# Performance work log

Measured on AMD Instinct MI355X. Metric: run time of the kernel, lower is better.

The kernel has to match this reference:

```python
import jax, jax.numpy as jnp
import numpy as np

B, S, D, H, DH = 4, 2048, 512, 8, 64

def setup_inputs() -> dict:
    key = jax.random.key(0)
    k1, k2, k3, k4 = jax.random.split(key, 4)
    sc = 1.0 / np.sqrt(D)
    return {
        "x": jax.random.normal(k1, (B, S, D), dtype=jnp.float32),
        "Wq": jax.random.normal(k2, (H, D, DH), dtype=jnp.float32) * sc,
        "Wk": jax.random.normal(k3, (H, D, DH), dtype=jnp.float32) * sc,
        "Wv": jax.random.normal(k4, (H, D, DH), dtype=jnp.float32) * sc,
    }

def reference(x, Wq, Wk, Wv):
    # x: [B,S,D]; Wq/Wk/Wv: [H,D,DH] (stacked per-head bias-free Linear weights)
    q = jnp.einsum('bsd,hdk->bhsk', x, Wq)
    k = jnp.einsum('bsd,hdk->bhsk', x, Wk)
    v = jnp.einsum('bsd,hdk->bhsk', x, Wv)
    scale = DH ** -0.5
    scores = jax.nn.softmax(jnp.einsum('bhqk,bhsk->bhqs', q, k) * scale, axis=-1)
    out = jnp.einsum('bhqs,bhsk->bhqk', scores, v)  # [B,H,S,DH]
    # concat heads along last dim (head order matches ModuleList order)
    return out.transpose(0, 2, 1, 3).reshape(B, S, H * DH)
```

## Files before the change

### kernel.cpp

```cpp
#include <hip/hip_runtime.h>

typedef _Float16 half8  __attribute__((ext_vector_type(8)));
typedef _Float16 half4v __attribute__((ext_vector_type(4)));
typedef _Float16 half2v __attribute__((ext_vector_type(2)));
typedef __fp16   fp16x2 __attribute__((ext_vector_type(2)));
typedef float    float4v __attribute__((ext_vector_type(4)));

#define CSC 0.18033688f

__device__ __forceinline__ void async16(const _Float16* g, void* l) {
    __builtin_amdgcn_global_load_lds((const __attribute__((address_space(1))) void*)g,
                                     (__attribute__((address_space(3))) void*)l, 16, 0, 0);
}

__device__ __forceinline__ half2v pk2(float a, float b) {
    return __builtin_bit_cast(half2v, __builtin_amdgcn_cvt_pkrtz(a, b));
}

__global__ __launch_bounds__(256) void mha_prep(const float* __restrict__ x,
    const float* __restrict__ wq, const float* __restrict__ wk, const float* __restrict__ wv,
    _Float16* __restrict__ xh, _Float16* __restrict__ wt) {
    __shared__ __align__(16) _Float16 T[64][72];
    const int tid = threadIdx.x;
    if (blockIdx.x < 4096) {
        int t = blockIdx.x * 256 + tid;
        float4v v = ((const float4v*)x)[t];
        half4v o;
        #pragma unroll
        for (int i = 0; i < 4; ++i) o[i] = (_Float16)v[i];
        ((half4v*)xh)[t] = o;
        return;
    }
    const int blk = blockIdx.x - 4096;
    const int dt = blk & 7, h = (blk >> 3) & 7, mat = blk >> 6;
    const float* w = ((mat == 0) ? wq : (mat == 1) ? wk : wv) + h * 32768 + dt * 64 * 64;
    #pragma unroll
    for (int i = 0; i < 4; ++i) {
        int s = tid + i * 256;
        int dl = s >> 4, c4 = s & 15;
        float4v v = ((const float4v*)(w + (size_t)dl * 64))[c4];
        #pragma unroll
        for (int e = 0; e < 4; ++e) T[c4 * 4 + e][dl] = (_Float16)v[e];
    }
    __syncthreads();
    #pragma unroll
    for (int i = 0; i < 2; ++i) {
        int s = tid + i * 256;
        int dh = s >> 3, c8 = s & 7;
        half8 o;
        #pragma unroll
        for (int e = 0; e < 8; ++e) o[e] = T[dh][c8 * 8 + e];
        *(half8*)(wt + (size_t)((mat * 8 + h) * 64 + dh) * 512 + dt * 64 + c8 * 8) = o;
    }
}

__global__ __launch_bounds__(256, 3) void mha_qkv(const _Float16* __restrict__ xh,
    const _Float16* __restrict__ wt, _Float16* __restrict__ Qm, _Float16* __restrict__ Km,
    _Float16* __restrict__ Vt) {
    __shared__ __align__(16) _Float16 Ash[2][128 * 32];
    __shared__ __align__(16) _Float16 Bsh[2][128 * 32];
    const int tid = threadIdx.x;
    const int lane = tid & 63, wave = tid >> 6;
    const int quad = lane >> 4, li = lane & 15;
    const int m0 = blockIdx.x * 128, n0 = blockIdx.y * 128;
    float4v acc[4][4] = {};
    const int r0 = tid >> 2, c0 = (tid & 3) ^ ((r0 >> 1) & 3);
    const int s1 = 256 + tid, r1 = s1 >> 2, c1 = (s1 & 3) ^ ((r1 >> 1) & 3);
    const _Float16* gA0 = xh + (size_t)(m0 + r0) * 512 + c0 * 8;
    const _Float16* gA1 = xh + (size_t)(m0 + r1) * 512 + c1 * 8;
    const _Float16* gB0 = wt + (size_t)(n0 + r0) * 512 + c0 * 8;
    const _Float16* gB1 = wt + (size_t)(n0 + r1) * 512 + c1 * 8;
    const int wr = (wave >> 1) * 64, wc = (wave & 1) * 64;
    const char* aB[2]; const char* bB[2];
    #pragma unroll
    for (int bb = 0; bb < 2; ++bb) {
        aB[bb] = (const char*)Ash[bb] + (wr + li) * 64 + ((quad ^ ((li >> 1) & 3)) << 4);
        bB[bb] = (const char*)Bsh[bb] + (wc + li) * 64 + ((quad ^ ((li >> 1) & 3)) << 4);
    }
    auto stage = [&](int bb, int kk) {
        async16(gA0 + kk, (char*)Ash[bb] + wave * 1024);
        async16(gA1 + kk, (char*)Ash[bb] + 4096 + wave * 1024);
        async16(gB0 + kk, (char*)Bsh[bb] + wave * 1024);
        async16(gB1 + kk, (char*)Bsh[bb] + 4096 + wave * 1024);
    };
    auto compute = [&](int bb) {
        half8 af[4], bf[4];
        #pragma unroll
        for (int mt = 0; mt < 4; ++mt) af[mt] = *(const half8*)(aB[bb] + mt * 1024);
        #pragma unroll
        for (int nt = 0; nt < 4; ++nt) bf[nt] = *(const half8*)(bB[bb] + nt * 1024);
        #pragma unroll
        for (int mt = 0; mt < 4; ++mt)
            #pragma unroll
            for (int nt = 0; nt < 4; ++nt)
                acc[mt][nt] = __builtin_amdgcn_mfma_f32_16x16x32_f16(af[mt], bf[nt], acc[mt][nt], 0, 0, 0);
    };
    stage(0, 0);
    for (int kk = 0; kk < 512; kk += 64) {
        __syncthreads();
        stage(1, kk + 32);
        compute(0);
        __syncthreads();
        if (kk + 64 < 512) stage(0, kk + 64);
        compute(1);
    }
    const int mat = n0 >> 9;
    const float osc = (mat == 0) ? CSC : 1.0f;
    #pragma unroll
    for (int mt = 0; mt < 4; ++mt) {
        int m = m0 + wr + mt * 16 + quad * 4;
        int b = m >> 11, s = m & 2047;
        #pragma unroll
        for (int nt = 0; nt < 4; ++nt) {
            int n = n0 + wc + nt * 16 + li;
            int h = (n >> 6) & 7, dh = n & 63;
            int bh = b * 8 + h;
            if (mat == 2) {
                half4v pkv;
                #pragma unroll
                for (int r = 0; r < 4; ++r) pkv[r] = (_Float16)acc[mt][nt][r];
                *(half4v*)(Vt + ((size_t)bh * 64 + dh) * 2048 + s) = pkv;
            } else {
                _Float16* dst = (mat == 0) ? Qm : Km;
                size_t base = ((size_t)bh * 2048 + s) * 64 + dh;
                #pragma unroll
                for (int r = 0; r < 4; ++r) dst[base + (size_t)r * 64] = (_Float16)(acc[mt][nt][r] * osc);
            }
        }
    }
}

__global__ __launch_bounds__(128, 2) void mha_attn(const _Float16* __restrict__ Qm,
    const _Float16* __restrict__ Km, const _Float16* __restrict__ Vt, float* __restrict__ out) {
    __shared__ __align__(16) _Float16 KtA[2][64 * 64];
    __shared__ __align__(16) _Float16 VtA[2][64 * 64];
    const int tid = threadIdx.x, lane = tid & 63, wave = tid >> 6;
    const int quad = lane >> 4, li = lane & 15;
    const int flat = blockIdx.x;
    const int qb = (flat >> 3) & 31;
    const int bh = ((flat >> 8) << 3) | (flat & 7);
    const int b = bh >> 3, h = bh & 7;
    const _Float16* Qg = Qm + (size_t)bh * 2048 * 64;
    const _Float16* Kg = Km + (size_t)bh * 2048 * 64;
    const _Float16* Vg = Vt + (size_t)bh * 64 * 2048;
    const int q0 = qb * 64 + wave * 32;
    half8 qf[2][2];
    #pragma unroll
    for (int qt = 0; qt < 2; ++qt)
        #pragma unroll
        for (int ds = 0; ds < 2; ++ds)
            qf[qt][ds] = *(const half8*)(Qg + (size_t)(q0 + qt * 16 + li) * 64 + ds * 32 + quad * 8);
    float4v O[2][4] = {};
    float lsum[2] = {0.f, 0.f};
    const _Float16* pK[4]; const _Float16* pV[4];
    #pragma unroll
    for (int is = 0; is < 4; ++is) {
        int s = is * 128 + tid;
        int rk = s >> 3, sck = s & 7;
        int swk = (rk & 3) | (((rk >> 3) & 1) << 2);
        int rv = s >> 3, cv = (s & 7) ^ (rv & 7);
        pK[is] = Kg + (size_t)rk * 64 + (sck ^ swk) * 8;
        pV[is] = Vg + (size_t)rv * 2048 + cv * 8;
    }
    auto stage = [&](int bb) {
        #pragma unroll
        for (int is = 0; is < 4; ++is) {
            async16(pK[is], (char*)KtA[bb] + is * 2048 + wave * 1024);
            async16(pV[is], (char*)VtA[bb] + is * 2048 + wave * 1024);
            pK[is] += 4096;
            pV[is] += 64;
        }
    };
    const int rowE = ((li >> 2) << 3) | (li & 3);
    const int swzE = (li & 3) | (((li >> 2) & 1) << 2);
    const char *k0e[2], *k1e[2], *vBq[2];
    #pragma unroll
    for (int bb = 0; bb < 2; ++bb) {
        const char* base = (const char*)KtA[bb] + rowE * 128;
        k0e[bb] = base + ((quad ^ swzE) << 4);
        k1e[bb] = base + (((quad + 4) ^ swzE) << 4);
        vBq[bb] = (const char*)VtA[bb] + li * 128;
    }
    int coff[2];
    #pragma unroll
    for (int c = 0; c < 2; ++c) coff[c] = (((c * 4 + quad) ^ (li & 7)) << 4);
    auto compute = [&](int bb) {
        #pragma unroll
        for (int c = 0; c < 2; ++c) {
            half8 f0e = *(const half8*)(k0e[bb] + c * 4096);
            half8 f1e = *(const half8*)(k1e[bb] + c * 4096);
            half8 f0o = *(const half8*)(k0e[bb] + c * 4096 + 512);
            half8 f1o = *(const half8*)(k1e[bb] + c * 4096 + 512);
            float4v se[2] = {}, so[2] = {};
            se[0] = __builtin_amdgcn_mfma_f32_16x16x32_f16(f0e, qf[0][0], se[0], 0, 0, 0);
            se[0] = __builtin_amdgcn_mfma_f32_16x16x32_f16(f1e, qf[0][1], se[0], 0, 0, 0);
            se[1] = __builtin_amdgcn_mfma_f32_16x16x32_f16(f0e, qf[1][0], se[1], 0, 0, 0);
            se[1] = __builtin_amdgcn_mfma_f32_16x16x32_f16(f1e, qf[1][1], se[1], 0, 0, 0);
            so[0] = __builtin_amdgcn_mfma_f32_16x16x32_f16(f0o, qf[0][0], so[0], 0, 0, 0);
            so[0] = __builtin_amdgcn_mfma_f32_16x16x32_f16(f1o, qf[0][1], so[0], 0, 0, 0);
            so[1] = __builtin_amdgcn_mfma_f32_16x16x32_f16(f0o, qf[1][0], so[1], 0, 0, 0);
            so[1] = __builtin_amdgcn_mfma_f32_16x16x32_f16(f1o, qf[1][1], so[1], 0, 0, 0);
            half8 pf[2];
            #pragma unroll
            for (int qt = 0; qt < 2; ++qt) {
                float pe[4], po[4];
                #pragma unroll
                for (int r = 0; r < 4; ++r) {
                    pe[r] = __builtin_amdgcn_exp2f(se[qt][r]);
                    po[r] = __builtin_amdgcn_exp2f(so[qt][r]);
                    lsum[qt] += pe[r] + po[r];
                }
                half4v a = __builtin_shufflevector(pk2(pe[0], pe[1]), pk2(pe[2], pe[3]), 0, 1, 2, 3);
                half4v o = __builtin_shufflevector(pk2(po[0], po[1]), pk2(po[2], po[3]), 0, 1, 2, 3);
                pf[qt] = __builtin_shufflevector(a, o, 0, 1, 2, 3, 4, 5, 6, 7);
            }
            #pragma unroll
            for (int dt = 0; dt < 4; ++dt) {
                half8 vf = *(const half8*)(vBq[bb] + dt * 2048 + coff[c]);
                O[0][dt] = __builtin_amdgcn_mfma_f32_16x16x32_f16(pf[0], vf, O[0][dt], 0, 0, 0);
                O[1][dt] = __builtin_amdgcn_mfma_f32_16x16x32_f16(pf[1], vf, O[1][dt], 0, 0, 0);
            }
        }
    };
    stage(0);
    for (int it = 0; it < 16; ++it) {
        __syncthreads();
        stage(1);
        compute(0);
        __syncthreads();
        if (it < 15) stage(0);
        compute(1);
    }
    #pragma unroll
    for (int qt = 0; qt < 2; ++qt) {
        float l = lsum[qt];
        l += __shfl_xor(l, 16);
        l += __shfl_xor(l, 32);
        #pragma unroll
        for (int r = 0; r < 4; ++r) {
            float lr = __shfl(l, quad * 4 + r);
            float inv = 1.0f / lr;
            int q = q0 + qt * 16 + quad * 4 + r;
            float* orow = out + ((size_t)(b * 2048 + q)) * 512 + h * 64;
            #pragma unroll
            for (int dt = 0; dt < 4; ++dt) orow[dt * 16 + li] = O[qt][dt][r] * inv;
        }
    }
}

extern "C" void kernel_launch(void* const* d_in, const int* in_sizes, int n_in,
                              void* d_out, int out_size, void* d_ws, size_t ws_size,
                              hipStream_t stream) {
    const float* x  = (const float*)d_in[0];
    const float* wq = (const float*)d_in[1];
    const float* wk = (const float*)d_in[2];
    const float* wv = (const float*)d_in[3];
    float* out = (float*)d_out;
    char* ws = (char*)d_ws;
    _Float16* xh = (_Float16*)(ws);
    _Float16* wt = (_Float16*)(ws + 8388608);
    _Float16* Qm = (_Float16*)(ws + 9961472);
    _Float16* Km = (_Float16*)(ws + 18350080);
    _Float16* Vt = (_Float16*)(ws + 26738688);
    if (ws_size < 35127296u) return;
    mha_prep<<<4288, 256, 0, stream>>>(x, wq, wk, wv, xh, wt);
    mha_qkv<<<dim3(64, 12), 256, 0, stream>>>(xh, wt, Qm, Km, Vt);
    mha_attn<<<1024, 128, 0, stream>>>(Qm, Km, Vt, out);
}
```

Baseline: 144.2 us.

## Split attention keys across two blocks with flag-based combine; stage Q/K epilogue via LDS

The attention kernel now uses 256-thread blocks covering 128 queries. Each block handles half of the key sequence. It writes unnormalized partial outputs and row sums to workspace, and the second block to finish (detected with an atomic counter) merges both halves and normalizes. Separately, the QKV GEMM epilogue for Q and K goes through an LDS transpose so the global stores are 16-byte vectors instead of scattered 2-byte writes. The split costs extra partial-output traffic, a memset and atomics. It relies on no max subtraction, since the scores are never shifted before exp2.

```diff
diff --git a/kernel.cpp b/kernel.cpp
--- a/kernel.cpp
+++ b/kernel.cpp
@@ -57,8 +57,9 @@
 __global__ __launch_bounds__(256, 3) void mha_qkv(const _Float16* __restrict__ xh,
     const _Float16* __restrict__ wt, _Float16* __restrict__ Qm, _Float16* __restrict__ Km,
     _Float16* __restrict__ Vt) {
-    __shared__ __align__(16) _Float16 Ash[2][128 * 32];
-    __shared__ __align__(16) _Float16 Bsh[2][128 * 32];
+    __shared__ __align__(16) char smem[34816];
+    _Float16* Ash[2] = { (_Float16*)smem,           (_Float16*)(smem + 8192)  };
+    _Float16* Bsh[2] = { (_Float16*)(smem + 16384), (_Float16*)(smem + 24576) };
     const int tid = threadIdx.x;
     const int lane = tid & 63, wave = tid >> 6;
     const int quad = lane >> 4, li = lane & 15;
@@ -105,45 +106,71 @@
         compute(1);
     }
     const int mat = n0 >> 9;
-    const float osc = (mat == 0) ? CSC : 1.0f;
-    #pragma unroll
-    for (int mt = 0; mt < 4; ++mt) {
-        int m = m0 + wr + mt * 16 + quad * 4;
-        int b = m >> 11, s = m & 2047;
-        #pragma unroll
-        for (int nt = 0; nt < 4; ++nt) {
-            int n = n0 + wc + nt * 16 + li;
-            int h = (n >> 6) & 7, dh = n & 63;
-            int bh = b * 8 + h;
-            if (mat == 2) {
+    if (mat == 2) {
+        #pragma unroll
+        for (int mt = 0; mt < 4; ++mt) {
+            int m = m0 + wr + mt * 16 + quad * 4;
+            int b = m >> 11, s = m & 2047;
+            #pragma unroll
+            for (int nt = 0; nt < 4; ++nt) {
+                int n = n0 + wc + nt * 16 + li;
+                int h = (n >> 6) & 7, dh = n & 63;
+                int bh = b * 8 + h;
                 half4v pkv;
                 #pragma unroll
                 for (int r = 0; r < 4; ++r) pkv[r] = (_Float16)acc[mt][nt][r];
                 *(half4v*)(Vt + ((size_t)bh * 64 + dh) * 2048 + s) = pkv;
-            } else {
-                _Float16* dst = (mat == 0) ? Qm : Km;
-                size_t base = ((size_t)bh * 2048 + s) * 64 + dh;
+            }
+        }
+    } else {
+        _Float16* dst = (mat == 0) ? Qm : Km;
+        const float osc = (mat == 0) ? CSC : 1.0f;
+        __syncthreads();
+        char* Tb = smem;
+        #pragma unroll
+        for (int mt = 0; mt < 4; ++mt) {
+            int rbase = wr + mt * 16 + quad * 4;
+            #pragma unroll
+            for (int nt = 0; nt < 4; ++nt) {
+                int col = wc + nt * 16 + li;
                 #pragma unroll
-                for (int r = 0; r < 4; ++r) dst[base + (size_t)r * 64] = (_Float16)(acc[mt][nt][r] * osc);
+                for (int r = 0; r < 4; ++r)
+                    *(_Float16*)(Tb + (rbase + r) * 272 + col * 2) = (_Float16)(acc[mt][nt][r] * osc);
             }
         }
-    }
-}
-
-__global__ __launch_bounds__(128, 2) void mha_attn(const _Float16* __restrict__ Qm,
-    const _Float16* __restrict__ Km, const _Float16* __restrict__ Vt, float* __restrict__ out) {
+        __syncthreads();
+        const int h0 = (n0 >> 6) & 7;
+        #pragma unroll
+        for (int i = 0; i < 8; ++i) {
+            int c = i * 256 + tid;
+            int row = c >> 4, j8 = c & 15;
+            half8 v = *(const half8*)(Tb + row * 272 + j8 * 16);
+            int m = m0 + row;
+            int b = m >> 11, s = m & 2047;
+            int bh = b * 8 + h0 + (j8 >> 3);
+            *(half8*)(dst + ((size_t)bh * 2048 + s) * 64 + (j8 & 7) * 8) = v;
+        }
+    }
+}
+
+__global__ __launch_bounds__(256, 4) void mha_attn(const _Float16* __restrict__ Qm,
+    const _Float16* __restrict__ Km, const _Float16* __restrict__ Vt,
+    float* __restrict__ opart, float* __restrict__ lpart, int* __restrict__ flags,
+    float* __restrict__ out) {
     __shared__ __align__(16) _Float16 KtA[2][64 * 64];
     __shared__ __align__(16) _Float16 VtA[2][64 * 64];
+    __shared__ int sflag;
     const int tid = threadIdx.x, lane = tid & 63, wave = tid >> 6;
     const int quad = lane >> 4, li = lane & 15;
     const int flat = blockIdx.x;
-    const int qb = (flat >> 3) & 31;
+    const int qb = (flat >> 3) & 15;
+    const int ks = (flat >> 7) & 1;
     const int bh = ((flat >> 8) << 3) | (flat & 7);
     const int b = bh >> 3, h = bh & 7;
     const _Float16* Qg = Qm + (size_t)bh * 2048 * 64;
-    const _Float16* Kg = Km + (size_t)bh * 2048 * 64;
-    const _Float16* Vg = Vt + (size_t)bh * 64 * 2048;
-    const int q0 = qb * 64 + wave * 32;
+    const _Float16* Kg = Km + (size_t)bh * 2048 * 64 + (size_t)ks * 1024 * 64;
+    const _Float16* Vg = Vt + (size_t)bh * 64 * 2048 + (size_t)ks * 1024;
+    const int q0 = qb * 128 + wave * 32;
     half8 qf[2][2];
     #pragma unroll
     for (int qt = 0; qt < 2; ++qt)
@@ -152,21 +179,21 @@
             qf[qt][ds] = *(const half8*)(Qg + (size_t)(q0 + qt * 16 + li) * 64 + ds * 32 + quad * 8);
     float4v O[2][4] = {};
     float lsum[2] = {0.f, 0.f};
-    const _Float16* pK[4]; const _Float16* pV[4];
-    #pragma unroll
-    for (int is = 0; is < 4; ++is) {
-        int s = is * 128 + tid;
-        int rk = s >> 3, sck = s & 7;
+    const _Float16* pK[2]; const _Float16* pV[2];
+    #pragma unroll
+    for (int is = 0; is < 2; ++is) {
+        int c = is * 256 + tid;
+        int rk = c >> 3, sck = c & 7;
         int swk = (rk & 3) | (((rk >> 3) & 1) << 2);
-        int rv = s >> 3, cv = (s & 7) ^ (rv & 7);
+        int cv = (c & 7) ^ (rk & 7);
         pK[is] = Kg + (size_t)rk * 64 + (sck ^ swk) * 8;
-        pV[is] = Vg + (size_t)rv * 2048 + cv * 8;
+        pV[is] = Vg + (size_t)rk * 2048 + cv * 8;
     }
     auto stage = [&](int bb) {
         #pragma unroll
-        for (int is = 0; is < 4; ++is) {
-            async16(pK[is], (char*)KtA[bb] + is * 2048 + wave * 1024);
-            async16(pV[is], (char*)VtA[bb] + is * 2048 + wave * 1024);
+        for (int is = 0; is < 2; ++is) {
+            async16(pK[is], (char*)KtA[bb] + is * 4096 + wave * 1024);
+            async16(pV[is], (char*)VtA[bb] + is * 4096 + wave * 1024);
             pK[is] += 4096;
             pV[is] += 64;
         }
@@ -176,9 +203,8 @@
     const char *k0e[2], *k1e[2], *vBq[2];
     #pragma unroll
     for (int bb = 0; bb < 2; ++bb) {
-        const char* base = (const char*)KtA[bb] + rowE * 128;
-        k0e[bb] = base + ((quad ^ swzE) << 4);
-        k1e[bb] = base + (((quad + 4) ^ swzE) << 4);
+        k0e[bb] = (const char*)KtA[bb] + rowE * 128 + ((quad ^ swzE) << 4);
+        k1e[bb] = (const char*)KtA[bb] + rowE * 128 + (((quad + 4) ^ swzE) << 4);
         vBq[bb] = (const char*)VtA[bb] + li * 128;
     }
     int coff[2];
@@ -223,27 +249,56 @@
         }
     };
     stage(0);
-    for (int it = 0; it < 16; ++it) {
+    for (int it = 0; it < 8; ++it) {
         __syncthreads();
         stage(1);
         compute(0);
         __syncthreads();
-        if (it < 15) stage(0);
+        if (it < 7) stage(0);
         compute(1);
     }
+    float lo[2];
     #pragma unroll
     for (int qt = 0; qt < 2; ++qt) {
         float l = lsum[qt];
         l += __shfl_xor(l, 16);
         l += __shfl_xor(l, 32);
+        lo[qt] = l;
+    }
+    float* obase = opart + (size_t)ks * 4194304;
+    #pragma unroll
+    for (int qt = 0; qt < 2; ++qt) {
+        #pragma unroll
+        for (int r = 0; r < 4; ++r) {
+            int q = q0 + qt * 16 + quad * 4 + r;
+            float* orow = obase + ((size_t)(b * 2048 + q)) * 512 + h * 64;
+            #pragma unroll
+            for (int dt = 0; dt < 4; ++dt) orow[dt * 16 + li] = O[qt][dt][r];
+        }
+        if (quad == 0) lpart[(size_t)ks * 65536 + bh * 2048 + q0 + qt * 16 + li] = lo[qt];
+    }
+    __threadfence();
+    __syncthreads();
+    if (tid == 0) sflag = atomicAdd(&flags[bh * 16 + qb], 1);
+    __syncthreads();
+    if (sflag == 0) return;
+    __threadfence();
+    const float* pbase = opart + (size_t)(1 - ks) * 4194304;
+    const float* plp = lpart + (size_t)(1 - ks) * 65536;
+    #pragma unroll
+    for (int qt = 0; qt < 2; ++qt) {
+        float l = lo[qt] + plp[bh * 2048 + q0 + qt * 16 + li];
         #pragma unroll
         for (int r = 0; r < 4; ++r) {
             float lr = __shfl(l, quad * 4 + r);
             float inv = 1.0f / lr;
             int q = q0 + qt * 16 + quad * 4 + r;
-            float* orow = out + ((size_t)(b * 2048 + q)) * 512 + h * 64;
-            #pragma unroll
-            for (int dt = 0; dt < 4; ++dt) orow[dt * 16 + li] = O[qt][dt][r] * inv;
+            size_t off = ((size_t)(b * 2048 + q)) * 512 + h * 64;
+            const float* prow = pbase + off;
+            float* orow = out + off;
+            #pragma unroll
+            for (int dt = 0; dt < 4; ++dt)
+                orow[dt * 16 + li] = (O[qt][dt][r] + prow[dt * 16 + li]) * inv;
         }
     }
 }
@@ -262,8 +317,12 @@
     _Float16* Qm = (_Float16*)(ws + 9961472);
     _Float16* Km = (_Float16*)(ws + 18350080);
     _Float16* Vt = (_Float16*)(ws + 26738688);
-    if (ws_size < 35127296u) return;
+    float* opart = (float*)(ws + 35127296);
+    float* lpart = (float*)(ws + 68681728);
+    int* flags   = (int*)(ws + 69206016);
+    if (ws_size < 69208064u) return;
+    hipMemsetAsync(flags, 0, 2048, stream);
     mha_prep<<<4288, 256, 0, stream>>>(x, wq, wk, wv, xh, wt);
     mha_qkv<<<dim3(64, 12), 256, 0, stream>>>(xh, wt, Qm, Km, Vt);
-    mha_attn<<<1024, 128, 0, stream>>>(Qm, Km, Vt, out);
-}
+    mha_attn<<<1024, 256, 0, stream>>>(Qm, Km, Vt, opart, lpart, flags, out);
+}
```

Result: slower. 321.1 us (+122.7%).
